# Kernel optimization log

Hardware: AMD Instinct MI355X
Metric: run time of the kernel (lower is better)

The kernel has to match this reference:

```python
import jax, jax.numpy as jnp
import numpy as np

N = 100000

def gcn_conv(x, W, b, src, dst, n):
    # PyG GCNConv: h = x W; add self-loops; norm = deg^-1/2[src]*deg^-1/2[dst]; scatter-add; + bias
    h = x @ W                                   # [N, out]
    deg = jax.ops.segment_sum(jnp.ones_like(dst, dtype=h.dtype), dst, num_segments=n)
    dinv = jnp.where(deg > 0, jax.lax.rsqrt(jnp.maximum(deg, 1e-12)), 0.0)
    norm = dinv[src] * dinv[dst]                # [E+N]
    msgs = h[src] * norm[:, None]               # gather + scale
    out = jax.ops.segment_sum(msgs, dst, num_segments=n)  # scatter-add
    return out + b

def setup_inputs() -> dict:
    key = jax.random.key(0)
    k1, k2, k3, k4, k5, k6 = jax.random.split(key, 6)
    E = 3200000
    F_in, H, C = 512, 50, 40
    x = jax.random.normal(k1, (N, F_in), dtype=jnp.float32)
    edge_index = jax.random.randint(k2, (2, E), 0, N, dtype=jnp.int32)
    # Glorot-style init for linear weights, zero bias (PyG default)
    W1 = jax.random.normal(k3, (F_in, H), dtype=jnp.float32) * (1.0 / np.sqrt(F_in))
    b1 = jnp.zeros((H,), dtype=jnp.float32)
    W2 = jax.random.normal(k4, (H, C), dtype=jnp.float32) * (1.0 / np.sqrt(H))
    b2 = jnp.zeros((C,), dtype=jnp.float32)
    return {"x": x, "W1": W1, "b1": b1, "W2": W2, "b2": b2, "edge_index": edge_index}

def reference(x, W1, b1, W2, b2, edge_index):
    n = x.shape[0]
    loops = jnp.arange(n, dtype=edge_index.dtype)
    src = jnp.concatenate([edge_index[0], loops])
    dst = jnp.concatenate([edge_index[1], loops])
    h = gcn_conv(x, W1, b1, src, dst, n)
    h = jax.nn.relu(h)
    # dropout identity in eval mode
    h = gcn_conv(h, W2, b2, src, dst, n)
    return jax.nn.log_softmax(h, axis=1)
```

## Files before the change

### kernel.cpp

```cpp
#include <hip/hip_runtime.h>
#include <hip/hip_bf16.h>
#include <math.h>

#define F_IN 512
#define H_DIM 50
#define C_DIM 40
#define ELL_W 80

typedef __bf16 bf16x8 __attribute__((ext_vector_type(8)));
typedef __bf16 bf16x4 __attribute__((ext_vector_type(4)));
typedef float f32x4 __attribute__((ext_vector_type(4)));


__global__ void zero_int_kernel(int* __restrict__ p, int n) {
    int i = blockIdx.x * blockDim.x + threadIdx.x;
    if (i < n) p[i] = 0;
}

__global__ void ell_fill_kernel(const int* __restrict__ src, const int* __restrict__ dst,
                                int* __restrict__ cnt, int* __restrict__ ell,
                                int E, int lo, int hi) {
    int e0 = (blockIdx.x * blockDim.x + threadIdx.x) * 4;
    if (e0 >= E) return;
    if (e0 + 3 < E) {
        int4 d4 = *(const int4*)(dst + e0);
        int4 s4 = *(const int4*)(src + e0);
        int dd[4] = {d4.x, d4.y, d4.z, d4.w};
        int ss[4] = {s4.x, s4.y, s4.z, s4.w};
        #pragma unroll
        for (int j = 0; j < 4; ++j) {
            int d = dd[j];
            if (d >= lo && d < hi) {
                int pos = atomicAdd(&cnt[d], 1);
                if (pos < ELL_W) ell[(long)d * ELL_W + pos] = ss[j];
            }
        }
    } else {
        for (int j = 0; j < 4 && e0 + j < E; ++j) {
            int d = dst[e0 + j];
            if (d >= lo && d < hi) {
                int pos = atomicAdd(&cnt[d], 1);
                if (pos < ELL_W) ell[(long)d * ELL_W + pos] = src[e0 + j];
            }
        }
    }
}

__global__ void dinv_kernel(const int* __restrict__ cnt, float* __restrict__ dinv, int N) {
    int i = blockIdx.x * blockDim.x + threadIdx.x;
    if (i < N) dinv[i] = rsqrtf((float)(cnt[i] + 1));
}


__global__ void prep_wt_kernel(const float* __restrict__ W1, __bf16* __restrict__ wt) {
    int i = blockIdx.x * 256 + threadIdx.x;
    int n = i >> 9, k = i & 511;
    wt[n * 512 + k] = (n < H_DIM) ? (__bf16)W1[k * H_DIM + n] : (__bf16)0.0f;
}


#define G1_BM 128
#define G1_BK 32
#define A_LDW 40

__device__ __forceinline__ bf16x4 pack4(float4 a) {
    bf16x4 r;
    r[0] = (__bf16)a.x; r[1] = (__bf16)a.y; r[2] = (__bf16)a.z; r[3] = (__bf16)a.w;
    return r;
}

__global__ __launch_bounds__(256) void gemm1_mfma_kernel(
    const float* __restrict__ x, const __bf16* __restrict__ wt,
    const float* __restrict__ dinv, __bf16* __restrict__ h1b, int N) {
    __shared__ __bf16 As[2][G1_BM * A_LDW];
    __shared__ __bf16 Bs[2][64 * A_LDW];

    const int t = threadIdx.x;
    const int wv = t >> 6, ln = t & 63;
    const int q = ln >> 4, l16 = ln & 15;
    const int row0 = blockIdx.x * G1_BM;

    f32x4 acc[2][4];
    #pragma unroll
    for (int a = 0; a < 2; ++a)
        #pragma unroll
        for (int b = 0; b < 4; ++b) acc[a][b] = (f32x4){0.f, 0.f, 0.f, 0.f};

    const int c4 = t & 7;
    const int r0 = t >> 3;
    const float* xp[4];
    #pragma unroll
    for (int j = 0; j < 4; ++j) {
        int gr = row0 + r0 + 32 * j;
        int rc = (gr < N) ? gr : (N - 1);
        xp[j] = x + (long)rc * F_IN + c4 * 4;
    }

    const int bc = t & 3;
    const int bn = t >> 2;
    const __bf16* wb = wt + bn * 512 + bc * 8;

    float4 xv[4];
    uint4 w8;

    #pragma unroll
    for (int j = 0; j < 4; ++j) xv[j] = *(const float4*)(xp[j]);
    w8 = *(const uint4*)(wb);
    #pragma unroll
    for (int j = 0; j < 4; ++j)
        *(bf16x4*)&As[0][(r0 + 32 * j) * A_LDW + c4 * 4] = pack4(xv[j]);
    *(bf16x8*)&Bs[0][bn * A_LDW + bc * 8] = *(bf16x8*)&w8;
    __syncthreads();

    #pragma unroll 1
    for (int tt = 0; tt < F_IN / G1_BK; ++tt) {
        int b = tt & 1;
        if (tt < F_IN / G1_BK - 1) {
            #pragma unroll
            for (int j = 0; j < 4; ++j)
                xv[j] = *(const float4*)(xp[j] + (tt + 1) * G1_BK);
            w8 = *(const uint4*)(wb + (tt + 1) * G1_BK);
        }
        bf16x8 af[2], bfr[4];
        #pragma unroll
        for (int mt = 0; mt < 2; ++mt)
            af[mt] = *(const bf16x8*)&As[b][(wv * 32 + mt * 16 + l16) * A_LDW + q * 8];
        #pragma unroll
        for (int nt = 0; nt < 4; ++nt)
            bfr[nt] = *(const bf16x8*)&Bs[b][(nt * 16 + l16) * A_LDW + q * 8];
        #pragma unroll
        for (int mt = 0; mt < 2; ++mt)
            #pragma unroll
            for (int nt = 0; nt < 4; ++nt)
                acc[mt][nt] = __builtin_amdgcn_mfma_f32_16x16x32_bf16(
                    af[mt], bfr[nt], acc[mt][nt], 0, 0, 0);
        if (tt < F_IN / G1_BK - 1) {
            int nb = b ^ 1;
            #pragma unroll
            for (int j = 0; j < 4; ++j)
                *(bf16x4*)&As[nb][(r0 + 32 * j) * A_LDW + c4 * 4] = pack4(xv[j]);
            *(bf16x8*)&Bs[nb][bn * A_LDW + bc * 8] = *(bf16x8*)&w8;
        }
        __syncthreads();
    }

    #pragma unroll
    for (int mt = 0; mt < 2; ++mt) {
        int rbase = row0 + wv * 32 + mt * 16 + q * 4;
        #pragma unroll
        for (int i = 0; i < 4; ++i) {
            int r = rbase + i;
            if (r < N) {
                float dv = dinv[r];
                #pragma unroll
                for (int nt = 0; nt < 4; ++nt)
                    h1b[(long)r * 64 + nt * 16 + l16] = (__bf16)(acc[mt][nt][i] * dv);
            }
        }
    }
}


__global__ __launch_bounds__(256) void gather1_gemm2_kernel(
    const int* __restrict__ cnt, const int* __restrict__ ell,
    const float* __restrict__ dinv, const __bf16* __restrict__ h1b,
    const float* __restrict__ b1, const float* __restrict__ W2,
    __bf16* __restrict__ h2b, int N) {
    __shared__ float w2s[H_DIM][C_DIM];
    __shared__ float b1s[64];
    __shared__ float r1s[4][64];
    for (int i = threadIdx.x; i < H_DIM * C_DIM; i += 256)
        w2s[i / C_DIM][i % C_DIM] = W2[i];
    if (threadIdx.x < 64)
        b1s[threadIdx.x] = (threadIdx.x < H_DIM) ? b1[threadIdx.x] : 0.0f;
    __syncthreads();

    const int lane = threadIdx.x & 63;
    const int wv = threadIdx.x >> 6;
    const int n = blockIdx.x * 4 + wv;
    const int c = lane & 7;
    const int g = lane >> 3;

    float acc[8];
    #pragma unroll
    for (int i = 0; i < 8; ++i) acc[i] = 0.0f;

    if (g == 0) {
        bf16x8 v = *(const bf16x8*)(h1b + (long)n * 64 + c * 8);
        #pragma unroll
        for (int i = 0; i < 8; ++i) acc[i] += (float)v[i];
    }

    const int c0 = min(cnt[n], ELL_W);
    const int* row = ell + (long)n * ELL_W;
    for (int base = 0; base < c0; base += 32) {
        int j0 = base + g, j1 = j0 + 8, j2 = j0 + 16, j3 = j0 + 24;
        bool p0 = j0 < c0, p1 = j1 < c0, p2 = j2 < c0, p3 = j3 < c0;
        int i0 = p0 ? row[j0] : n;
        int i1 = p1 ? row[j1] : n;
        int i2 = p2 ? row[j2] : n;
        int i3 = p3 ? row[j3] : n;
        bf16x8 v0 = *(const bf16x8*)(h1b + (long)i0 * 64 + c * 8);
        bf16x8 v1 = *(const bf16x8*)(h1b + (long)i1 * 64 + c * 8);
        bf16x8 v2 = *(const bf16x8*)(h1b + (long)i2 * 64 + c * 8);
        bf16x8 v3 = *(const bf16x8*)(h1b + (long)i3 * 64 + c * 8);
        float m0 = p0 ? 1.f : 0.f, m1 = p1 ? 1.f : 0.f;
        float m2 = p2 ? 1.f : 0.f, m3 = p3 ? 1.f : 0.f;
        #pragma unroll
        for (int i = 0; i < 8; ++i) {
            acc[i] = fmaf(m0, (float)v0[i], acc[i]);
            acc[i] = fmaf(m1, (float)v1[i], acc[i]);
            acc[i] = fmaf(m2, (float)v2[i], acc[i]);
            acc[i] = fmaf(m3, (float)v3[i], acc[i]);
        }
    }

    #pragma unroll
    for (int i = 0; i < 8; ++i) {
        acc[i] += __shfl_xor(acc[i], 8, 64);
        acc[i] += __shfl_xor(acc[i], 16, 64);
        acc[i] += __shfl_xor(acc[i], 32, 64);
    }
    const float dv = dinv[n];
    if (g == 0) {
        #pragma unroll
        for (int i = 0; i < 8; ++i)
            r1s[wv][c * 8 + i] = fmaxf(acc[i] * dv + b1s[c * 8 + i], 0.0f);
    }
    __syncthreads();

    float h2 = 0.0f;
    if (lane < C_DIM) {
        float a2 = 0.0f;
        #pragma unroll
        for (int k = 0; k < H_DIM; ++k) a2 += r1s[wv][k] * w2s[k][lane];
        h2 = a2 * dv;
    }
    h2b[(long)n * 64 + lane] = (lane < C_DIM) ? (__bf16)h2 : (__bf16)0.0f;
}


__global__ __launch_bounds__(256) void gather2_kernel(
    const int* __restrict__ cnt, const int* __restrict__ ell,
    const float* __restrict__ dinv, const __bf16* __restrict__ h2b,
    const float* __restrict__ b2, float* __restrict__ out2, int N) {
    __shared__ float sc[4][64];
    const int lane = threadIdx.x & 63;
    const int wv = threadIdx.x >> 6;
    const int n = blockIdx.x * 4 + wv;
    const int c = lane & 7;
    const int g = lane >> 3;

    float acc[8];
    #pragma unroll
    for (int i = 0; i < 8; ++i) acc[i] = 0.0f;

    if (g == 0) {
        bf16x8 v = *(const bf16x8*)(h2b + (long)n * 64 + c * 8);
        #pragma unroll
        for (int i = 0; i < 8; ++i) acc[i] += (float)v[i];
    }

    const int c0 = min(cnt[n], ELL_W);
    const int* row = ell + (long)n * ELL_W;
    for (int base = 0; base < c0; base += 32) {
        int j0 = base + g, j1 = j0 + 8, j2 = j0 + 16, j3 = j0 + 24;
        bool p0 = j0 < c0, p1 = j1 < c0, p2 = j2 < c0, p3 = j3 < c0;
        int i0 = p0 ? row[j0] : n;
        int i1 = p1 ? row[j1] : n;
        int i2 = p2 ? row[j2] : n;
        int i3 = p3 ? row[j3] : n;
        bf16x8 v0 = *(const bf16x8*)(h2b + (long)i0 * 64 + c * 8);
        bf16x8 v1 = *(const bf16x8*)(h2b + (long)i1 * 64 + c * 8);
        bf16x8 v2 = *(const bf16x8*)(h2b + (long)i2 * 64 + c * 8);
        bf16x8 v3 = *(const bf16x8*)(h2b + (long)i3 * 64 + c * 8);
        float m0 = p0 ? 1.f : 0.f, m1 = p1 ? 1.f : 0.f;
        float m2 = p2 ? 1.f : 0.f, m3 = p3 ? 1.f : 0.f;
        #pragma unroll
        for (int i = 0; i < 8; ++i) {
            acc[i] = fmaf(m0, (float)v0[i], acc[i]);
            acc[i] = fmaf(m1, (float)v1[i], acc[i]);
            acc[i] = fmaf(m2, (float)v2[i], acc[i]);
            acc[i] = fmaf(m3, (float)v3[i], acc[i]);
        }
    }

    #pragma unroll
    for (int i = 0; i < 8; ++i) {
        acc[i] += __shfl_xor(acc[i], 8, 64);
        acc[i] += __shfl_xor(acc[i], 16, 64);
        acc[i] += __shfl_xor(acc[i], 32, 64);
    }
    if (g == 0) {
        #pragma unroll
        for (int i = 0; i < 8; ++i) sc[wv][c * 8 + i] = acc[i];
    }
    __syncthreads();

    const bool valid = lane < C_DIM;
    float v = valid ? (sc[wv][lane] * dinv[n] + b2[lane]) : -INFINITY;

    float m = v;
    #pragma unroll
    for (int off = 1; off < 64; off <<= 1)
        m = fmaxf(m, __shfl_xor(m, off, 64));
    float ex = valid ? __expf(v - m) : 0.0f;
    #pragma unroll
    for (int off = 1; off < 64; off <<= 1)
        ex += __shfl_xor(ex, off, 64);
    float ls = __logf(ex) + m;
    if (valid) out2[(long)n * C_DIM + lane] = v - ls;
}


extern "C" void kernel_launch(void* const* d_in, const int* in_sizes, int n_in,
                              void* d_out, int out_size, void* d_ws, size_t ws_size,
                              hipStream_t stream) {
    const float* x  = (const float*)d_in[0];
    const float* W1 = (const float*)d_in[1];
    const float* b1 = (const float*)d_in[2];
    const float* W2 = (const float*)d_in[3];
    const float* b2 = (const float*)d_in[4];
    const int* ei   = (const int*)d_in[5];

    const int N = in_sizes[0] / F_IN;
    const int E = in_sizes[5] / 2;
    const int* src = ei;
    const int* dst = ei + E;
    float* out2 = (float*)d_out;

    int* wsw = (int*)d_ws;
    long o = 0;
    int*    cnt  = wsw + o;  o += N;
    int*    ell  = wsw + o;  o += (long)N * ELL_W;
    float*  dinv = (float*)(wsw + o); o += N;
    __bf16* wt   = (__bf16*)(wsw + o); o += (64 * 512) / 2;
    __bf16* h1b  = (__bf16*)(wsw + o); o += (long)N * 32;
    __bf16* h2b  = (__bf16*)(wsw + o); o += (long)N * 32;

    const int BT = 256;
    const int gN = (N + BT - 1) / BT;
    const int gE4 = (E / 4 + BT - 1) / BT;

    zero_int_kernel<<<gN, BT, 0, stream>>>(cnt, N);
    const int P = 4;
    for (int p = 0; p < P; ++p) {
        int lo = (int)((long)N * p / P);
        int hi = (int)((long)N * (p + 1) / P);
        ell_fill_kernel<<<gE4, BT, 0, stream>>>(src, dst, cnt, ell, E, lo, hi);
    }
    dinv_kernel<<<gN, BT, 0, stream>>>(cnt, dinv, N);
    prep_wt_kernel<<<128, 256, 0, stream>>>(W1, wt);

    gemm1_mfma_kernel<<<(N + G1_BM - 1) / G1_BM, 256, 0, stream>>>(x, wt, dinv, h1b, N);
    gather1_gemm2_kernel<<<N / 4, 256, 0, stream>>>(cnt, ell, dinv, h1b, b1, W2, h2b, N);
    gather2_kernel<<<N / 4, 256, 0, stream>>>(cnt, ell, dinv, h2b, b2, out2, N);
}
```

Measured before the change: 663.7 us.

## Replace multi-pass ELL adjacency build with count-scan-fill CSR construction

Builds a compact CSR adjacency via a degree count, a three-kernel prefix scan, and a single atomic-cursor fill pass, replacing four partitioned ELL fill passes over all edges. This cuts repeated edge reads and the padded 80-wide ELL storage, and removes the degree truncation. It adds extra small scan launches and an extra atomic pass for counting.

```diff
diff --git a/kernel.cpp b/kernel.cpp
--- a/kernel.cpp
+++ b/kernel.cpp
@@ -5,7 +5,6 @@
 #define F_IN 512
 #define H_DIM 50
 #define C_DIM 40
-#define ELL_W 80
 
 typedef __bf16 bf16x8 __attribute__((ext_vector_type(8)));
 typedef __bf16 bf16x4 __attribute__((ext_vector_type(4)));
@@ -17,9 +16,86 @@
     if (i < n) p[i] = 0;
 }
 
-__global__ void ell_fill_kernel(const int* __restrict__ src, const int* __restrict__ dst,
-                                int* __restrict__ cnt, int* __restrict__ ell,
-                                int E, int lo, int hi) {
+__global__ void count_kernel(const int* __restrict__ dst, int* __restrict__ cnt, int E) {
+    int e0 = (blockIdx.x * blockDim.x + threadIdx.x) * 4;
+    if (e0 >= E) return;
+    if (e0 + 3 < E) {
+        int4 d4 = *(const int4*)(dst + e0);
+        atomicAdd(&cnt[d4.x], 1);
+        atomicAdd(&cnt[d4.y], 1);
+        atomicAdd(&cnt[d4.z], 1);
+        atomicAdd(&cnt[d4.w], 1);
+    } else {
+        for (int j = 0; j < 4 && e0 + j < E; ++j) atomicAdd(&cnt[dst[e0 + j]], 1);
+    }
+}
+
+__global__ __launch_bounds__(256) void scan1_kernel(
+    const int* __restrict__ cnt, int* __restrict__ rowptr,
+    int* __restrict__ blksum, int N) {
+    __shared__ int wsum[4];
+    const int t = threadIdx.x, lane = t & 63, wv = t >> 6;
+    const int base = blockIdx.x * 1024 + t * 4;
+    int v[4];
+    #pragma unroll
+    for (int j = 0; j < 4; ++j) v[j] = (base + j < N) ? cnt[base + j] : 0;
+    int tsum = v[0] + v[1] + v[2] + v[3];
+    int incl = tsum;
+    #pragma unroll
+    for (int off = 1; off < 64; off <<= 1) {
+        int u = __shfl_up(incl, off, 64);
+        if (lane >= off) incl += u;
+    }
+    if (lane == 63) wsum[wv] = incl;
+    __syncthreads();
+    int woff = 0;
+    #pragma unroll
+    for (int w = 0; w < 3; ++w) woff += (w < wv) ? wsum[w] : 0;
+    int e = woff + incl - tsum;
+    #pragma unroll
+    for (int j = 0; j < 4; ++j) {
+        if (base + j < N) rowptr[base + j] = e;
+        e += v[j];
+    }
+    if (t == 255) blksum[blockIdx.x] = woff + incl;
+}
+
+__global__ void scan2_kernel(int* __restrict__ blksum, int nb) {
+    const int lane = threadIdx.x;
+    int run = 0;
+    for (int base = 0; base < nb; base += 64) {
+        int v = (base + lane < nb) ? blksum[base + lane] : 0;
+        int incl = v;
+        #pragma unroll
+        for (int off = 1; off < 64; off <<= 1) {
+            int u = __shfl_up(incl, off, 64);
+            if (lane >= off) incl += u;
+        }
+        if (base + lane < nb) blksum[base + lane] = run + incl - v;
+        run += __shfl(incl, 63, 64);
+    }
+}
+
+__global__ __launch_bounds__(256) void scan3_kernel(
+    int* __restrict__ rowptr, const int* __restrict__ blksum,
+    int* __restrict__ cursor, const int* __restrict__ cnt,
+    float* __restrict__ dinv, int N) {
+    const int base = blockIdx.x * 1024 + threadIdx.x * 4;
+    const int off = blksum[blockIdx.x];
+    #pragma unroll
+    for (int j = 0; j < 4; ++j) {
+        int i = base + j;
+        if (i < N) {
+            int r = rowptr[i] + off;
+            rowptr[i] = r;
+            cursor[i] = r;
+            dinv[i] = rsqrtf((float)(cnt[i] + 1));
+        }
+    }
+}
+
+__global__ void csr_fill_kernel(const int* __restrict__ src, const int* __restrict__ dst,
+                                int* __restrict__ cursor, int* __restrict__ adj, int E) {
     int e0 = (blockIdx.x * blockDim.x + threadIdx.x) * 4;
     if (e0 >= E) return;
     if (e0 + 3 < E) {
@@ -29,26 +105,15 @@
         int ss[4] = {s4.x, s4.y, s4.z, s4.w};
         #pragma unroll
         for (int j = 0; j < 4; ++j) {
-            int d = dd[j];
-            if (d >= lo && d < hi) {
-                int pos = atomicAdd(&cnt[d], 1);
-                if (pos < ELL_W) ell[(long)d * ELL_W + pos] = ss[j];
-            }
+            int pos = atomicAdd(&cursor[dd[j]], 1);
+            adj[pos] = ss[j];
         }
     } else {
         for (int j = 0; j < 4 && e0 + j < E; ++j) {
-            int d = dst[e0 + j];
-            if (d >= lo && d < hi) {
-                int pos = atomicAdd(&cnt[d], 1);
-                if (pos < ELL_W) ell[(long)d * ELL_W + pos] = src[e0 + j];
-            }
-        }
-    }
-}
-
-__global__ void dinv_kernel(const int* __restrict__ cnt, float* __restrict__ dinv, int N) {
-    int i = blockIdx.x * blockDim.x + threadIdx.x;
-    if (i < N) dinv[i] = rsqrtf((float)(cnt[i] + 1));
+            int pos = atomicAdd(&cursor[dst[e0 + j]], 1);
+            adj[pos] = src[e0 + j];
+        }
+    }
 }
 
 
@@ -162,7 +227,8 @@
 
 
 __global__ __launch_bounds__(256) void gather1_gemm2_kernel(
-    const int* __restrict__ cnt, const int* __restrict__ ell,
+    const int* __restrict__ rowptr, const int* __restrict__ cnt,
+    const int* __restrict__ adj,
     const float* __restrict__ dinv, const __bf16* __restrict__ h1b,
     const float* __restrict__ b1, const float* __restrict__ W2,
     __bf16* __restrict__ h2b, int N) {
@@ -191,8 +257,8 @@
         for (int i = 0; i < 8; ++i) acc[i] += (float)v[i];
     }
 
-    const int c0 = min(cnt[n], ELL_W);
-    const int* row = ell + (long)n * ELL_W;
+    const int c0 = cnt[n];
+    const int* row = adj + rowptr[n];
     for (int base = 0; base < c0; base += 32) {
         int j0 = base + g, j1 = j0 + 8, j2 = j0 + 16, j3 = j0 + 24;
         bool p0 = j0 < c0, p1 = j1 < c0, p2 = j2 < c0, p3 = j3 < c0;
@@ -241,7 +307,8 @@
 
 
 __global__ __launch_bounds__(256) void gather2_kernel(
-    const int* __restrict__ cnt, const int* __restrict__ ell,
+    const int* __restrict__ rowptr, const int* __restrict__ cnt,
+    const int* __restrict__ adj,
     const float* __restrict__ dinv, const __bf16* __restrict__ h2b,
     const float* __restrict__ b2, float* __restrict__ out2, int N) {
     __shared__ float sc[4][64];
@@ -261,8 +328,8 @@
         for (int i = 0; i < 8; ++i) acc[i] += (float)v[i];
     }
 
-    const int c0 = min(cnt[n], ELL_W);
-    const int* row = ell + (long)n * ELL_W;
+    const int c0 = cnt[n];
+    const int* row = adj + rowptr[n];
     for (int base = 0; base < c0; base += 32) {
         int j0 = base + g, j1 = j0 + 8, j2 = j0 + 16, j3 = j0 + 24;
         bool p0 = j0 < c0, p1 = j1 < c0, p2 = j2 < c0, p3 = j3 < c0;
@@ -331,28 +398,30 @@
 
     int* wsw = (int*)d_ws;
     long o = 0;
-    int*    cnt  = wsw + o;  o += N;
-    int*    ell  = wsw + o;  o += (long)N * ELL_W;
-    float*  dinv = (float*)(wsw + o); o += N;
-    __bf16* wt   = (__bf16*)(wsw + o); o += (64 * 512) / 2;
-    __bf16* h1b  = (__bf16*)(wsw + o); o += (long)N * 32;
-    __bf16* h2b  = (__bf16*)(wsw + o); o += (long)N * 32;
+    int*    cnt    = wsw + o;  o += N;
+    int*    rowptr = wsw + o;  o += N;
+    int*    cursor = wsw + o;  o += N;
+    int*    blksum = wsw + o;  o += 1024;
+    int*    adj    = wsw + o;  o += E;
+    float*  dinv   = (float*)(wsw + o); o += N;
+    __bf16* wt     = (__bf16*)(wsw + o); o += (64 * 512) / 2;
+    __bf16* h1b    = (__bf16*)(wsw + o); o += (long)N * 32;
+    __bf16* h2b    = (__bf16*)(wsw + o); o += (long)N * 32;
 
     const int BT = 256;
-    const int gN = (N + BT - 1) / BT;
-    const int gE4 = (E / 4 + BT - 1) / BT;
+    const int gN   = (N + BT - 1) / BT;
+    const int gE4  = (E / 4 + BT - 1) / BT;
+    const int gS   = (N + 1023) / 1024;
 
     zero_int_kernel<<<gN, BT, 0, stream>>>(cnt, N);
-    const int P = 4;
-    for (int p = 0; p < P; ++p) {
-        int lo = (int)((long)N * p / P);
-        int hi = (int)((long)N * (p + 1) / P);
-        ell_fill_kernel<<<gE4, BT, 0, stream>>>(src, dst, cnt, ell, E, lo, hi);
-    }
-    dinv_kernel<<<gN, BT, 0, stream>>>(cnt, dinv, N);
+    count_kernel<<<gE4, BT, 0, stream>>>(dst, cnt, E);
+    scan1_kernel<<<gS, BT, 0, stream>>>(cnt, rowptr, blksum, N);
+    scan2_kernel<<<1, 64, 0, stream>>>(blksum, gS);
+    scan3_kernel<<<gS, BT, 0, stream>>>(rowptr, blksum, cursor, cnt, dinv, N);
+    csr_fill_kernel<<<gE4, BT, 0, stream>>>(src, dst, cursor, adj, E);
     prep_wt_kernel<<<128, 256, 0, stream>>>(W1, wt);
 
     gemm1_mfma_kernel<<<(N + G1_BM - 1) / G1_BM, 256, 0, stream>>>(x, wt, dinv, h1b, N);
-    gather1_gemm2_kernel<<<N / 4, 256, 0, stream>>>(cnt, ell, dinv, h1b, b1, W2, h2b, N);
-    gather2_kernel<<<N / 4, 256, 0, stream>>>(cnt, ell, dinv, h2b, b2, out2, N);
-}
+    gather1_gemm2_kernel<<<N / 4, 256, 0, stream>>>(rowptr, cnt, adj, dinv, h1b, b1, W2, h2b, N);
+    gather2_kernel<<<N / 4, 256, 0, stream>>>(rowptr, cnt, adj, dinv, h2b, b2, out2, N);
+}
```

Measured after the change: 866.9 us. 30.6% more time.

## Replace atomic ELL fill with two-pass bucketed CSR construction

Applied to the files above, without the earlier changes.

Replaces the four-pass, global-atomic ELL adjacency fill with a bucket partition by destination block, using shared-memory atomics and one global atomic per bucket per block. A second kernel then builds per-bucket CSR with a local histogram and scan, and computes degree and dinv in the same pass. The gather kernels switch from fixed-width ELL rows to rowptr/adj. This removes the contended global atomics and the ELL width cap, but relies on a fixed per-bucket capacity of twice the average, which silently drops edges if a bucket overflows.

```diff
diff --git a/kernel.cpp b/kernel.cpp
--- a/kernel.cpp
+++ b/kernel.cpp
@@ -5,50 +5,116 @@
 #define F_IN 512
 #define H_DIM 50
 #define C_DIM 40
-#define ELL_W 80
+#define NB_SHIFT 9
+#define NB_SIZE (1 << NB_SHIFT)
+#define PB_EDGES 4096
 
 typedef __bf16 bf16x8 __attribute__((ext_vector_type(8)));
 typedef __bf16 bf16x4 __attribute__((ext_vector_type(4)));
 typedef float f32x4 __attribute__((ext_vector_type(4)));
 
 
-__global__ void zero_int_kernel(int* __restrict__ p, int n) {
-    int i = blockIdx.x * blockDim.x + threadIdx.x;
-    if (i < n) p[i] = 0;
-}
-
-__global__ void ell_fill_kernel(const int* __restrict__ src, const int* __restrict__ dst,
-                                int* __restrict__ cnt, int* __restrict__ ell,
-                                int E, int lo, int hi) {
-    int e0 = (blockIdx.x * blockDim.x + threadIdx.x) * 4;
-    if (e0 >= E) return;
-    if (e0 + 3 < E) {
-        int4 d4 = *(const int4*)(dst + e0);
-        int4 s4 = *(const int4*)(src + e0);
-        int dd[4] = {d4.x, d4.y, d4.z, d4.w};
-        int ss[4] = {s4.x, s4.y, s4.z, s4.w};
-        #pragma unroll
-        for (int j = 0; j < 4; ++j) {
-            int d = dd[j];
-            if (d >= lo && d < hi) {
-                int pos = atomicAdd(&cnt[d], 1);
-                if (pos < ELL_W) ell[(long)d * ELL_W + pos] = ss[j];
+__global__ void init_bcur_kernel(int* __restrict__ bcur, int cap) {
+    bcur[threadIdx.x] = threadIdx.x * cap;
+}
+
+__global__ __launch_bounds__(256) void partition_kernel(
+    const int* __restrict__ src, const int* __restrict__ dst,
+    int* __restrict__ bcur, int* __restrict__ ebuf, int E, int cap) {
+    __shared__ int lcnt[256];
+    __shared__ int lbase[256];
+    const int t = threadIdx.x;
+    lcnt[t] = 0;
+    __syncthreads();
+    const long b0 = (long)blockIdx.x * PB_EDGES;
+    int s[16], d[16], rk[16];
+    #pragma unroll
+    for (int ci = 0; ci < 4; ++ci) {
+        long e = b0 + ci * 1024 + t * 4;
+        const int j0 = ci * 4;
+        if (e + 3 < E) {
+            int4 d4 = *(const int4*)(dst + e);
+            int4 s4 = *(const int4*)(src + e);
+            s[j0] = s4.x; s[j0 + 1] = s4.y; s[j0 + 2] = s4.z; s[j0 + 3] = s4.w;
+            d[j0] = d4.x; d[j0 + 1] = d4.y; d[j0 + 2] = d4.z; d[j0 + 3] = d4.w;
+        } else {
+            #pragma unroll
+            for (int j = 0; j < 4; ++j) {
+                if (e + j < E) { s[j0 + j] = src[e + j]; d[j0 + j] = dst[e + j]; }
+                else           { s[j0 + j] = 0;          d[j0 + j] = -1; }
             }
         }
-    } else {
-        for (int j = 0; j < 4 && e0 + j < E; ++j) {
-            int d = dst[e0 + j];
-            if (d >= lo && d < hi) {
-                int pos = atomicAdd(&cnt[d], 1);
-                if (pos < ELL_W) ell[(long)d * ELL_W + pos] = src[e0 + j];
-            }
-        }
-    }
-}
-
-__global__ void dinv_kernel(const int* __restrict__ cnt, float* __restrict__ dinv, int N) {
-    int i = blockIdx.x * blockDim.x + threadIdx.x;
-    if (i < N) dinv[i] = rsqrtf((float)(cnt[i] + 1));
+        #pragma unroll
+        for (int j = 0; j < 4; ++j)
+            rk[j0 + j] = (d[j0 + j] >= 0) ? atomicAdd(&lcnt[d[j0 + j] >> NB_SHIFT], 1) : -1;
+    }
+    __syncthreads();
+    lbase[t] = lcnt[t] ? atomicAdd(&bcur[t], lcnt[t]) : 0;
+    __syncthreads();
+    #pragma unroll
+    for (int j = 0; j < 16; ++j)
+        if (rk[j] >= 0) {
+            int bk = d[j] >> NB_SHIFT;
+            int idx = lbase[bk] + rk[j];
+            if (idx < (bk + 1) * cap)
+                ebuf[idx] = (s[j] << NB_SHIFT) | (d[j] & (NB_SIZE - 1));
+        }
+}
+
+__global__ __launch_bounds__(256) void bucket_csr_kernel(
+    const int* __restrict__ ebuf, const int* __restrict__ bcur,
+    int* __restrict__ cnt, int* __restrict__ rowptr, float* __restrict__ dinv,
+    int* __restrict__ adj, int N, int cap) {
+    __shared__ int h[NB_SIZE];
+    __shared__ int wsum[4];
+    const int t = threadIdx.x, lane = t & 63, wv = t >> 6;
+    const int b = blockIdx.x, v0 = b << NB_SHIFT;
+    const int gbase = b * cap;
+    const int cb = min(bcur[b] - gbase, cap);
+    h[2 * t] = 0; h[2 * t + 1] = 0;
+    __syncthreads();
+    const int* ep = ebuf + gbase;
+    for (int i = t; i < cb; i += 256)
+        atomicAdd(&h[ep[i] & (NB_SIZE - 1)], 1);
+    __syncthreads();
+    const int a0 = h[2 * t], a1 = h[2 * t + 1];
+    const int tsum = a0 + a1;
+    int incl = tsum;
+    #pragma unroll
+    for (int off = 1; off < 64; off <<= 1) {
+        int u = __shfl_up(incl, off, 64);
+        if (lane >= off) incl += u;
+    }
+    if (lane == 63) wsum[wv] = incl;
+    __syncthreads();
+    int woff = 0;
+    #pragma unroll
+    for (int w = 0; w < 3; ++w) woff += (w < wv) ? wsum[w] : 0;
+    const int ex = woff + incl - tsum;
+    const int r0 = gbase + ex, r1 = r0 + a0;
+    h[2 * t] = r0; h[2 * t + 1] = r1;
+    const int i0 = v0 + 2 * t, i1 = i0 + 1;
+    if (i0 < N) { rowptr[i0] = r0; cnt[i0] = a0; dinv[i0] = rsqrtf((float)(a0 + 1)); }
+    if (i1 < N) { rowptr[i1] = r1; cnt[i1] = a1; dinv[i1] = rsqrtf((float)(a1 + 1)); }
+    __syncthreads();
+    const int nq = cb >> 2;
+    for (int q = t; q < nq; q += 256) {
+        int4 e4 = *(const int4*)(ep + q * 4);
+        int p0 = atomicAdd(&h[e4.x & (NB_SIZE - 1)], 1);
+        int p1 = atomicAdd(&h[e4.y & (NB_SIZE - 1)], 1);
+        int p2 = atomicAdd(&h[e4.z & (NB_SIZE - 1)], 1);
+        int p3 = atomicAdd(&h[e4.w & (NB_SIZE - 1)], 1);
+        adj[p0] = e4.x >> NB_SHIFT;
+        adj[p1] = e4.y >> NB_SHIFT;
+        adj[p2] = e4.z >> NB_SHIFT;
+        adj[p3] = e4.w >> NB_SHIFT;
+    }
+    const int rem = cb & 3;
+    if (t < rem) {
+        int e = ep[nq * 4 + t];
+        int p = atomicAdd(&h[e & (NB_SIZE - 1)], 1);
+        adj[p] = e >> NB_SHIFT;
+    }
 }
 
 
@@ -162,7 +228,8 @@
 
 
 __global__ __launch_bounds__(256) void gather1_gemm2_kernel(
-    const int* __restrict__ cnt, const int* __restrict__ ell,
+    const int* __restrict__ rowptr, const int* __restrict__ cnt,
+    const int* __restrict__ adj,
     const float* __restrict__ dinv, const __bf16* __restrict__ h1b,
     const float* __restrict__ b1, const float* __restrict__ W2,
     __bf16* __restrict__ h2b, int N) {
@@ -191,8 +258,8 @@
         for (int i = 0; i < 8; ++i) acc[i] += (float)v[i];
     }
 
-    const int c0 = min(cnt[n], ELL_W);
-    const int* row = ell + (long)n * ELL_W;
+    const int c0 = cnt[n];
+    const int* row = adj + rowptr[n];
     for (int base = 0; base < c0; base += 32) {
         int j0 = base + g, j1 = j0 + 8, j2 = j0 + 16, j3 = j0 + 24;
         bool p0 = j0 < c0, p1 = j1 < c0, p2 = j2 < c0, p3 = j3 < c0;
@@ -241,7 +308,8 @@
 
 
 __global__ __launch_bounds__(256) void gather2_kernel(
-    const int* __restrict__ cnt, const int* __restrict__ ell,
+    const int* __restrict__ rowptr, const int* __restrict__ cnt,
+    const int* __restrict__ adj,
     const float* __restrict__ dinv, const __bf16* __restrict__ h2b,
     const float* __restrict__ b2, float* __restrict__ out2, int N) {
     __shared__ float sc[4][64];
@@ -261,8 +329,8 @@
         for (int i = 0; i < 8; ++i) acc[i] += (float)v[i];
     }
 
-    const int c0 = min(cnt[n], ELL_W);
-    const int* row = ell + (long)n * ELL_W;
+    const int c0 = cnt[n];
+    const int* row = adj + rowptr[n];
     for (int base = 0; base < c0; base += 32) {
         int j0 = base + g, j1 = j0 + 8, j2 = j0 + 16, j3 = j0 + 24;
         bool p0 = j0 < c0, p1 = j1 < c0, p2 = j2 < c0, p3 = j3 < c0;
@@ -329,30 +397,30 @@
     const int* dst = ei + E;
     float* out2 = (float*)d_out;
 
+    const int nbuck = (N + NB_SIZE - 1) >> NB_SHIFT;
+    const int CAP = (int)((((long)2 * E / nbuck) + 255) & ~255L);
+
     int* wsw = (int*)d_ws;
     long o = 0;
-    int*    cnt  = wsw + o;  o += N;
-    int*    ell  = wsw + o;  o += (long)N * ELL_W;
-    float*  dinv = (float*)(wsw + o); o += N;
-    __bf16* wt   = (__bf16*)(wsw + o); o += (64 * 512) / 2;
-    __bf16* h1b  = (__bf16*)(wsw + o); o += (long)N * 32;
-    __bf16* h2b  = (__bf16*)(wsw + o); o += (long)N * 32;
+    int*    cnt    = wsw + o;  o += N;
+    int*    bcur   = wsw + o;  o += 256;
+    int*    rowptr = wsw + o;  o += N;
+    int*    adj    = wsw + o;  o += (long)nbuck * CAP;
+    int*    ebuf   = wsw + o;  o += (long)nbuck * CAP;
+    float*  dinv   = (float*)(wsw + o); o += N;
+    __bf16* wt     = (__bf16*)(wsw + o); o += (64 * 512) / 2;
+    __bf16* h1b    = (__bf16*)(wsw + o); o += (long)N * 32;
+    __bf16* h2b    = (__bf16*)(wsw + o); o += (long)N * 32;
 
     const int BT = 256;
-    const int gN = (N + BT - 1) / BT;
-    const int gE4 = (E / 4 + BT - 1) / BT;
-
-    zero_int_kernel<<<gN, BT, 0, stream>>>(cnt, N);
-    const int P = 4;
-    for (int p = 0; p < P; ++p) {
-        int lo = (int)((long)N * p / P);
-        int hi = (int)((long)N * (p + 1) / P);
-        ell_fill_kernel<<<gE4, BT, 0, stream>>>(src, dst, cnt, ell, E, lo, hi);
-    }
-    dinv_kernel<<<gN, BT, 0, stream>>>(cnt, dinv, N);
+    const int gP = (E + PB_EDGES - 1) / PB_EDGES;
+
+    init_bcur_kernel<<<1, 256, 0, stream>>>(bcur, CAP);
+    partition_kernel<<<gP, BT, 0, stream>>>(src, dst, bcur, ebuf, E, CAP);
+    bucket_csr_kernel<<<nbuck, BT, 0, stream>>>(ebuf, bcur, cnt, rowptr, dinv, adj, N, CAP);
     prep_wt_kernel<<<128, 256, 0, stream>>>(W1, wt);
 
     gemm1_mfma_kernel<<<(N + G1_BM - 1) / G1_BM, 256, 0, stream>>>(x, wt, dinv, h1b, N);
-    gather1_gemm2_kernel<<<N / 4, 256, 0, stream>>>(cnt, ell, dinv, h1b, b1, W2, h2b, N);
-    gather2_kernel<<<N / 4, 256, 0, stream>>>(cnt, ell, dinv, h2b, b2, out2, N);
-}
+    gather1_gemm2_kernel<<<N / 4, 256, 0, stream>>>(rowptr, cnt, adj, dinv, h1b, b1, W2, h2b, N);
+    gather2_kernel<<<N / 4, 256, 0, stream>>>(rowptr, cnt, adj, dinv, h2b, b2, out2, N);
+}
```

Result: faster. 539.1 us (-18.8%).
